# Performance work log

Measured on AMD Instinct MI355X. Metric: run time of the kernel, lower is better.

Reference implementation:

```python
import jax, jax.numpy as jnp
import numpy as np


def setup_inputs() -> dict:
    key = jax.random.key(0)
    k1, k2, k3 = jax.random.split(key, 3)
    B, C_IN, C_OUT, R, K = 4, 64, 64, 64, 3
    x = jax.random.normal(k1, (B, C_IN, R, R, R), dtype=jnp.float32)
    # per-voxel nonzero test |x|.sum(channel) != 0 used by the module)
    keep = jax.random.uniform(k2, (B, 1, R, R, R)) < 0.3
    x = x * keep.astype(jnp.float32)
    weight = jax.random.normal(k3, (C_OUT, C_IN, K, K, K), dtype=jnp.float32)
    return {"x": x, "weight": weight}


def reference(x, weight):
    # The torch module gathers a k^3 neighborhood at every nonzero input voxel,
    # contracts with the (unflipped) weight, and scatters to the same voxel.
    # This is exactly cross-correlation (torch conv semantics) with SAME padding,
    # masked to voxels where the input is nonzero across channels.
    K = weight.shape[-1]
    pad_l = K // 2
    pad_r = K - 1 - pad_l
    out = jax.lax.conv_general_dilated(
        x, weight,
        window_strides=(1, 1, 1),
        padding=[(pad_l, pad_r)] * 3,
        dimension_numbers=("NCDHW", "OIDHW", "NCDHW"),
    )  # [B, C_out, D, H, W]
    mask = (jnp.abs(x).sum(axis=1, keepdims=True) != 0)  # [B,1,D,H,W]
    return out * mask.astype(out.dtype)
```

## Files before the change

kernel.cpp:

```cpp
#include <hip/hip_runtime.h>
#include <stdint.h>


#define R3 262144
#define NVOX (4 * R3)
#define P  66
#define PS (66 * 66)
#define PB (66 * 66 * 66)
#define WSW_ELEMS (27 * 2 * 4 * 64 * 8)
#define CAP (NVOX / 2)

typedef __attribute__((ext_vector_type(4))) float f32x4;
typedef __attribute__((ext_vector_type(8))) short short8;

static __device__ inline unsigned short f2bf(float f) {
    union { float f; unsigned u; } v; v.f = f;
    unsigned u = v.u;
    return (unsigned short)((u + 0x7fffu + ((u >> 16) & 1u)) >> 16);
}

static __device__ __forceinline__ void gload16(const void* g, void* l) {
    __builtin_amdgcn_global_load_lds(
        (const __attribute__((address_space(1))) unsigned int*)g,
        (__attribute__((address_space(3))) unsigned int*)l, 16, 0, 0);
}

__global__ void wprep(const float* __restrict__ w, unsigned short* __restrict__ wsw) {
    int e = blockIdx.x * 256 + threadIdx.x;
    if (e >= WSW_ELEMS) return;
    int j    = e & 7;
    int lane = (e >> 3) & 63;
    int nt   = (e >> 9) & 3;
    int kc   = (e >> 11) & 1;
    int tap  = e >> 12;
    int co = nt * 16 + (lane & 15);
    int ci = kc * 32 + ((lane >> 4) * 8) + j;
    wsw[e] = f2bf(w[(co * 64 + ci) * 27 + tap]);
}

__global__ void __launch_bounds__(256) halo_zero(uint4* __restrict__ xt4) {
    int p = blockIdx.x * 256 + threadIdx.x;
    if (p >= 4 * PB) return;
    int b = p / PB;
    int rp = p - b * PB;
    int z = rp / PS; rp -= z * PS;
    int y = rp / P;  int xx = rp - y * P;
    if (z == 0 || z == 65 || y == 0 || y == 65 || xx == 0 || xx == 65) {
        uint4 zz = {0, 0, 0, 0};
        uint4* d = xt4 + (size_t)p * 8;
#pragma unroll
        for (int k = 0; k < 8; ++k) d[k] = zz;
    }
}

__global__ void __launch_bounds__(256) xprep(const float* __restrict__ x,
                                             unsigned int* __restrict__ xt_u32,
                                             int* __restrict__ list,
                                             int* __restrict__ pos,
                                             int* __restrict__ count) {
    __shared__ unsigned int lds[256 * 36];
    __shared__ unsigned int wcnt[4], wbase[4], bbase;
    int t = threadIdx.x;
    int v = blockIdx.x * 256 + t;
    int b = v >> 18;
    int s = v & (R3 - 1);
    const float* xb = x + (size_t)b * (64 * R3) + s;
    bool active = false;
    unsigned int pk[32];
#pragma unroll
    for (int c2 = 0; c2 < 32; ++c2) {
        float f0 = xb[(size_t)(2 * c2) * R3];
        float f1 = xb[(size_t)(2 * c2 + 1) * R3];
        active |= (f0 != 0.f) | (f1 != 0.f);
        pk[c2] = (unsigned)f2bf(f0) | ((unsigned)f2bf(f1) << 16);
    }
#pragma unroll
    for (int k = 0; k < 8; ++k) {
        uint4 q = { pk[4 * k], pk[4 * k + 1], pk[4 * k + 2], pk[4 * k + 3] };
        *(uint4*)&lds[t * 36 + 4 * k] = q;
    }
    __syncthreads();
    int s0 = (blockIdx.x * 256) & (R3 - 1);
    int z0 = s0 >> 12;
    int y0 = (s0 >> 6) & 63;
    size_t rowbase = ((size_t)b * PB + (size_t)(z0 + 1) * PS + (size_t)(y0 + 1) * P + 1) * 32;
#pragma unroll
    for (int i = 0; i < 8; ++i) {
        int g4 = i * 256 + t;
        int vox = g4 >> 3;
        int col = (g4 & 7) * 4;
        uint4 val = *(const uint4*)&lds[vox * 36 + col];
        int r = vox >> 6;
        int xc = vox & 63;
        *(uint4*)&xt_u32[rowbase + (size_t)r * (P * 32) + (size_t)xc * 32 + col] = val;
    }
    int lane = t & 63, w = t >> 6;
    unsigned long long bal = __ballot(active);
    if (lane == 0) wcnt[w] = (unsigned)__popcll(bal);
    __syncthreads();
    if (t == 0) {
        unsigned tot = 0;
        for (int i = 0; i < 4; ++i) { wbase[i] = tot; tot += wcnt[i]; }
        bbase = (unsigned)atomicAdd(count, (int)tot);
    }
    __syncthreads();
    int p = -1;
    if (active) {
        unsigned pp = bbase + wbase[w] + (unsigned)__popcll(bal & ((1ULL << lane) - 1ULL));
        list[pp] = v;
        p = (int)pp;
    }
    pos[v] = p;
}

#define STAGE(tap, buf) do {                                                       \
    const int dz_ = (tap) / 9 - 1, dy_ = ((tap) / 3) % 3 - 1, dx_ = (tap) % 3 - 1; \
    const ptrdiff_t dlt_ = (ptrdiff_t)(dz_ * PS + dy_ * P + dx_) * 128;            \
    _Pragma("unroll")                                                              \
    for (int i_ = 0; i_ < 4; ++i_)                                                 \
        gload16(asrc[i_] + dlt_, &Ab[buf][t * 16 + i_ * 8192]);                    \
    gload16(wswb + (size_t)(tap) * 8192 + t * 16, &Bb[buf][t * 16]);               \
} while (0)

__global__ void __launch_bounds__(512) sconv_gemm(const unsigned char* __restrict__ xt,
                                                  const unsigned char* __restrict__ wswb,
                                                  const int* __restrict__ list,
                                                  const int* __restrict__ count_p,
                                                  float* __restrict__ out,
                                                  float* __restrict__ compact,
                                                  int use_compact) {
    __shared__ __align__(16) unsigned char Ab[2][32768];
    __shared__ __align__(16) unsigned char Bb[2][8192];
    int count = *count_p;
    int nt_act = (count + 255) >> 8;
    int bid = blockIdx.x;
    if (bid >= nt_act) return;
    int qd = nt_act >> 3, rd = nt_act & 7;
    int xcd = bid & 7, ixx = bid >> 3;
    int tile = (xcd < rd ? xcd * (qd + 1) : rd * (qd + 1) + (xcd - rd) * qd) + ixx;
    int base = tile * 256;
    int t = threadIdx.x;

    const unsigned char* asrc[4];
    {
        int seg = t & 7;
        int r0 = t >> 3;
        int off = (seg * 16) ^ ((r0 & 7) << 4);
#pragma unroll
        for (int i = 0; i < 4; ++i) {
            int gi = base + r0 + 64 * i;
            int vid = (gi < count) ? list[gi] : 0;
            if (vid < 0) vid = 0;
            int bb = vid >> 18, sp = vid & (R3 - 1);
            int vz = sp >> 12, vy = (sp >> 6) & 63, vx = sp & 63;
            size_t pvox = (size_t)bb * PB + (size_t)(vz + 1) * PS + (size_t)(vy + 1) * P + (vx + 1);
            asrc[i] = xt + pvox * 128 + off;
        }
    }

    int lane = t & 63, w = t >> 6;
    int cl = lane & 15;
    int hi16 = (lane >> 4) * 16;
    int aswz = (cl & 7) << 4;
    int aoff[2][2];
#pragma unroll
    for (int m = 0; m < 2; ++m)
#pragma unroll
        for (int kc = 0; kc < 2; ++kc)
            aoff[m][kc] = (w * 32 + m * 16 + cl) * 128 + ((kc * 64 + hi16) ^ aswz);
    int boff[2][4];
#pragma unroll
    for (int kc = 0; kc < 2; ++kc)
#pragma unroll
        for (int n = 0; n < 4; ++n)
            boff[kc][n] = ((kc * 4 + n) * 64 + lane) * 16;

    f32x4 acc[2][4] = {};

    STAGE(0, 0);
#pragma unroll
    for (int tap = 0; tap < 27; ++tap) {
        const int cur = tap & 1;
        asm volatile("s_waitcnt vmcnt(0)" ::: "memory");
        asm volatile("s_barrier" ::: "memory");
        if (tap < 26) { STAGE(tap + 1, cur ^ 1); }
#pragma unroll
        for (int kc = 0; kc < 2; ++kc) {
            short8 a0 = *(const short8*)&Ab[cur][aoff[0][kc]];
            short8 a1 = *(const short8*)&Ab[cur][aoff[1][kc]];
#pragma unroll
            for (int n = 0; n < 4; ++n) {
                short8 bf = *(const short8*)&Bb[cur][boff[kc][n]];
                acc[0][n] = __builtin_amdgcn_mfma_f32_16x16x32_bf16(a0, bf, acc[0][n], 0, 0, 0);
                acc[1][n] = __builtin_amdgcn_mfma_f32_16x16x32_bf16(a1, bf, acc[1][n], 0, 0, 0);
            }
        }
        asm volatile("s_waitcnt lgkmcnt(0)" ::: "memory");
    }

    int q = lane >> 4;
    if (use_compact) {
#pragma unroll
        for (int m = 0; m < 2; ++m) {
#pragma unroll
            for (int rg = 0; rg < 4; ++rg) {
                int row = w * 32 + m * 16 + q * 4 + rg;
                int gi = base + row;
                if (gi < count && gi < CAP) {
#pragma unroll
                    for (int n = 0; n < 4; ++n)
                        compact[(size_t)gi * 64 + n * 16 + cl] = acc[m][n][rg];
                }
            }
        }
    } else {
#pragma unroll
        for (int m = 0; m < 2; ++m) {
#pragma unroll
            for (int rg = 0; rg < 4; ++rg) {
                int row = w * 32 + m * 16 + q * 4 + rg;
                int gi = base + row;
                if (gi < count) {
                    int vv = list[gi];
                    int bb2 = vv >> 18;
                    int sp = vv & (R3 - 1);
                    float* op = out + (size_t)(bb2 * 64 + cl) * R3 + sp;
#pragma unroll
                    for (int n = 0; n < 4; ++n)
                        op[(size_t)(n * 16) * R3] = acc[m][n][rg];
                }
            }
        }
    }
}

__global__ void __launch_bounds__(256) finalize(const uint4* __restrict__ compact4,
                                                const int* __restrict__ pos,
                                                float* __restrict__ out) {
    int t = threadIdx.x;
    int vb = blockIdx.x * 256;
    int b = vb >> 18;
    int sp0 = vb & (R3 - 1);
    int q = pos[vb + t];
    bool act = (unsigned)q < (unsigned)CAP;
    const uint4* src = compact4 + (size_t)(act ? q : 0) * 16;
    uint4 r[16];
#pragma unroll
    for (int s = 0; s < 16; ++s) {
        uint4 v = {0, 0, 0, 0};
        if (act) v = src[s];
        r[s] = v;
    }
    const float* rf = (const float*)r;
    float* ob = out + (size_t)b * 64 * R3 + sp0 + t;
#pragma unroll
    for (int co = 0; co < 64; ++co)
        ob[(size_t)co * R3] = rf[co];
}

__global__ void __launch_bounds__(64) fallback_conv(const float* __restrict__ x,
                                                    const float* __restrict__ wt,
                                                    float* __restrict__ out) {
    __shared__ float rowb[66];
    int bid = blockIdx.x;
    int y = bid & 63, z = (bid >> 6) & 63, co = (bid >> 12) & 63, b = bid >> 18;
    int t = threadIdx.x;
    float acc = 0.f;
    bool active = false;
    for (int ci = 0; ci < 64; ++ci) {
        const float* xp = x + ((size_t)(b * 64 + ci)) * R3;
        const float* wp = wt + ((size_t)(co * 64 + ci)) * 27;
        for (int dz = -1; dz <= 1; ++dz) {
            int nz = z + dz;
            bool okz = (unsigned)nz < 64u;
            for (int dy = -1; dy <= 1; ++dy) {
                int ny = y + dy;
                bool ok = okz && ((unsigned)ny < 64u);
                float v = ok ? xp[nz * 4096 + ny * 64 + t] : 0.f;
                rowb[t + 1] = v;
                if (t == 0) { rowb[0] = 0.f; rowb[65] = 0.f; }
                __syncthreads();
                if (dz == 0 && dy == 0) active |= (rowb[t + 1] != 0.f);
                const float* wq = wp + (dz + 1) * 9 + (dy + 1) * 3;
                acc += rowb[t] * wq[0] + rowb[t + 1] * wq[1] + rowb[t + 2] * wq[2];
                __syncthreads();
            }
        }
    }
    out[((size_t)(b * 64 + co)) * R3 + z * 4096 + y * 64 + t] = active ? acc : 0.f;
}

extern "C" void kernel_launch(void* const* d_in, const int* in_sizes, int n_in,
                              void* d_out, int out_size, void* d_ws, size_t ws_size,
                              hipStream_t stream) {
    const float* x = (const float*)d_in[0];
    const float* w = (const float*)d_in[1];
    float* out = (float*)d_out;

    const size_t XT_BYTES = (size_t)4 * PB * 128;
    const size_t LIST_OFF = XT_BYTES;
    const size_t POS_OFF  = LIST_OFF + (size_t)NVOX * 4;
    const size_t WSW_OFF  = POS_OFF + (size_t)NVOX * 4;
    const size_t CNT_OFF  = WSW_OFF + (size_t)WSW_ELEMS * 2;
    const size_t CMP_OFF  = (CNT_OFF + 256 + 255) & ~(size_t)255;
    const size_t NEED_S   = CMP_OFF;
    const size_t NEED_C   = CMP_OFF + (size_t)CAP * 64 * 4;

    if (ws_size < NEED_S) {
        fallback_conv<<<NVOX, 64, 0, stream>>>(x, w, out);
        return;
    }

    unsigned int*   xt   = (unsigned int*)d_ws;
    int*            list = (int*)((char*)d_ws + LIST_OFF);
    int*            pos  = (int*)((char*)d_ws + POS_OFF);
    unsigned short* wsw  = (unsigned short*)((char*)d_ws + WSW_OFF);
    int*            cnt  = (int*)((char*)d_ws + CNT_OFF);
    float*          cmp  = (float*)((char*)d_ws + CMP_OFF);
    int use_compact = (ws_size >= NEED_C) ? 1 : 0;

    hipMemsetAsync(cnt, 0, sizeof(int), stream);
    if (!use_compact)
        hipMemsetAsync(d_out, 0, (size_t)out_size * sizeof(float), stream);
    wprep<<<WSW_ELEMS / 256, 256, 0, stream>>>(w, wsw);
    halo_zero<<<(4 * PB + 255) / 256, 256, 0, stream>>>((uint4*)d_ws);
    xprep<<<NVOX / 256, 256, 0, stream>>>(x, xt, list, pos, cnt);
    sconv_gemm<<<NVOX / 256, 512, 0, stream>>>((const unsigned char*)xt,
                                               (const unsigned char*)wsw, list, cnt,
                                               out, cmp, use_compact);
    if (use_compact)
        finalize<<<NVOX / 256, 256, 0, stream>>>((const uint4*)cmp, pos, out);
}
```

Before: 650.8 us.

## Restructure sparse conv GEMM into per-wave triple-buffered pipeline with register-held weights

Each wave now stages its own 32-row A tile into a private 3-slot LDS ring and loads B (weights) straight from global into double-buffered registers. Block-level barriers are replaced with vmcnt-based waits. Blocks shrink to 256 threads and 128 voxels, with a 3-blocks-per-CU launch bound. The goal is to remove the per-tap barrier stalls and overlap global loads with MFMA work. The cost is that every wave fetches the weights separately, raising register pressure and global weight traffic.

Result: slower. 683.0 us (+4.9%).

```diff
diff --git a/kernel.cpp b/kernel.cpp
--- a/kernel.cpp
+++ b/kernel.cpp
@@ -113,42 +113,50 @@
     pos[v] = p;
 }
 
-#define STAGE(tap, buf) do {                                                       \
-    const int dz_ = (tap) / 9 - 1, dy_ = ((tap) / 3) % 3 - 1, dx_ = (tap) % 3 - 1; \
-    const ptrdiff_t dlt_ = (ptrdiff_t)(dz_ * PS + dy_ * P + dx_) * 128;            \
-    _Pragma("unroll")                                                              \
-    for (int i_ = 0; i_ < 4; ++i_)                                                 \
-        gload16(asrc[i_] + dlt_, &Ab[buf][t * 16 + i_ * 8192]);                    \
-    gload16(wswb + (size_t)(tap) * 8192 + t * 16, &Bb[buf][t * 16]);               \
-} while (0)
-
-__global__ void __launch_bounds__(512) sconv_gemm(const unsigned char* __restrict__ xt,
-                                                  const unsigned char* __restrict__ wswb,
-                                                  const int* __restrict__ list,
-                                                  const int* __restrict__ count_p,
-                                                  float* __restrict__ out,
-                                                  float* __restrict__ compact,
-                                                  int use_compact) {
-    __shared__ __align__(16) unsigned char Ab[2][32768];
-    __shared__ __align__(16) unsigned char Bb[2][8192];
+#define AST(tp, sl) do { if ((tp) < 27) {                                           \
+    const int dz_ = (tp) / 9 - 1, dy_ = ((tp) / 3) % 3 - 1, dx_ = (tp) % 3 - 1;     \
+    const ptrdiff_t dlt_ = (ptrdiff_t)(dz_ * PS + dy_ * P + dx_) * 128;             \
+    _Pragma("unroll")                                                               \
+    for (int i_ = 0; i_ < 4; ++i_)                                                  \
+        gload16(asrc[i_] + dlt_, aw + (sl) * 4096 + i_ * 1024 + lane * 16);         \
+    asm volatile("" ::: "memory");                                                  \
+} } while (0)
+
+#define BLD(tp, st) do { if ((tp) < 27) {                                           \
+    _Pragma("unroll")                                                               \
+    for (int j_ = 0; j_ < 8; ++j_)                                                  \
+        breg[st][j_] = *(const short8*)(wswb + (size_t)(tp) * 8192 + j_ * 1024      \
+                                        + lane * 16);                               \
+    asm volatile("" ::: "memory");                                                  \
+} } while (0)
+
+__global__ void __launch_bounds__(256, 3) sconv_gemm(const unsigned char* __restrict__ xt,
+                                                     const unsigned char* __restrict__ wswb,
+                                                     const int* __restrict__ list,
+                                                     const int* __restrict__ count_p,
+                                                     float* __restrict__ out,
+                                                     float* __restrict__ compact,
+                                                     int use_compact) {
+    __shared__ __align__(16) unsigned char Ab[4][3][4096];
     int count = *count_p;
-    int nt_act = (count + 255) >> 8;
+    int nt_act = (count + 127) >> 7;
     int bid = blockIdx.x;
     if (bid >= nt_act) return;
     int qd = nt_act >> 3, rd = nt_act & 7;
     int xcd = bid & 7, ixx = bid >> 3;
     int tile = (xcd < rd ? xcd * (qd + 1) : rd * (qd + 1) + (xcd - rd) * qd) + ixx;
-    int base = tile * 256;
+    int base = tile * 128;
     int t = threadIdx.x;
+    int lane = t & 63, w = t >> 6;
 
     const unsigned char* asrc[4];
     {
-        int seg = t & 7;
-        int r0 = t >> 3;
-        int off = (seg * 16) ^ ((r0 & 7) << 4);
+        int seg = lane & 7;
+        int rl0 = lane >> 3;
+        int off = (seg * 16) ^ ((rl0 & 7) << 4);
 #pragma unroll
         for (int i = 0; i < 4; ++i) {
-            int gi = base + r0 + 64 * i;
+            int gi = base + w * 32 + rl0 + 8 * i;
             int vid = (gi < count) ? list[gi] : 0;
             if (vid < 0) vid = 0;
             int bb = vid >> 18, sp = vid & (R3 - 1);
@@ -157,43 +165,45 @@
             asrc[i] = xt + pvox * 128 + off;
         }
     }
-
-    int lane = t & 63, w = t >> 6;
+    unsigned char* aw = &Ab[w][0][0];
+
     int cl = lane & 15;
     int hi16 = (lane >> 4) * 16;
-    int aswz = (cl & 7) << 4;
     int aoff[2][2];
 #pragma unroll
     for (int m = 0; m < 2; ++m)
 #pragma unroll
         for (int kc = 0; kc < 2; ++kc)
-            aoff[m][kc] = (w * 32 + m * 16 + cl) * 128 + ((kc * 64 + hi16) ^ aswz);
-    int boff[2][4];
-#pragma unroll
-    for (int kc = 0; kc < 2; ++kc)
-#pragma unroll
-        for (int n = 0; n < 4; ++n)
-            boff[kc][n] = ((kc * 4 + n) * 64 + lane) * 16;
+            aoff[m][kc] = (m * 16 + cl) * 128 + ((kc * 64 + hi16) ^ ((cl & 7) << 4));
 
     f32x4 acc[2][4] = {};
-
-    STAGE(0, 0);
-#pragma unroll
-    for (int tap = 0; tap < 27; ++tap) {
-        const int cur = tap & 1;
-        asm volatile("s_waitcnt vmcnt(0)" ::: "memory");
-        asm volatile("s_barrier" ::: "memory");
-        if (tap < 26) { STAGE(tap + 1, cur ^ 1); }
-#pragma unroll
-        for (int kc = 0; kc < 2; ++kc) {
-            short8 a0 = *(const short8*)&Ab[cur][aoff[0][kc]];
-            short8 a1 = *(const short8*)&Ab[cur][aoff[1][kc]];
-#pragma unroll
-            for (int n = 0; n < 4; ++n) {
-                short8 bf = *(const short8*)&Bb[cur][boff[kc][n]];
-                acc[0][n] = __builtin_amdgcn_mfma_f32_16x16x32_bf16(a0, bf, acc[0][n], 0, 0, 0);
-                acc[1][n] = __builtin_amdgcn_mfma_f32_16x16x32_bf16(a1, bf, acc[1][n], 0, 0, 0);
-            }
+    short8 breg[2][8];
+
+    BLD(0, 0);
+    AST(0, 0);
+    AST(1, 1);
+#pragma unroll
+    for (int tp = 0; tp < 27; ++tp) {
+        const int sl = tp % 3;
+        const int st = tp & 1;
+        if (tp == 0)       asm volatile("s_waitcnt vmcnt(4)"  ::: "memory");
+        else if (tp < 26)  asm volatile("s_waitcnt vmcnt(12)" ::: "memory");
+        else               asm volatile("s_waitcnt vmcnt(8)"  ::: "memory");
+        short8 a0k0 = *(const short8*)(aw + sl * 4096 + aoff[0][0]);
+        short8 a1k0 = *(const short8*)(aw + sl * 4096 + aoff[1][0]);
+        short8 a0k1 = *(const short8*)(aw + sl * 4096 + aoff[0][1]);
+        short8 a1k1 = *(const short8*)(aw + sl * 4096 + aoff[1][1]);
+        BLD(tp + 1, st ^ 1);
+        AST(tp + 2, (tp + 2) % 3);
+#pragma unroll
+        for (int n = 0; n < 4; ++n) {
+            acc[0][n] = __builtin_amdgcn_mfma_f32_16x16x32_bf16(a0k0, breg[st][n], acc[0][n], 0, 0, 0);
+            acc[1][n] = __builtin_amdgcn_mfma_f32_16x16x32_bf16(a1k0, breg[st][n], acc[1][n], 0, 0, 0);
+        }
+#pragma unroll
+        for (int n = 0; n < 4; ++n) {
+            acc[0][n] = __builtin_amdgcn_mfma_f32_16x16x32_bf16(a0k1, breg[st][4 + n], acc[0][n], 0, 0, 0);
+            acc[1][n] = __builtin_amdgcn_mfma_f32_16x16x32_bf16(a1k1, breg[st][4 + n], acc[1][n], 0, 0, 0);
         }
         asm volatile("s_waitcnt lgkmcnt(0)" ::: "memory");
     }
@@ -325,7 +335,7 @@
     wprep<<<WSW_ELEMS / 256, 256, 0, stream>>>(w, wsw);
     halo_zero<<<(4 * PB + 255) / 256, 256, 0, stream>>>((uint4*)d_ws);
     xprep<<<NVOX / 256, 256, 0, stream>>>(x, xt, list, pos, cnt);
-    sconv_gemm<<<NVOX / 256, 512, 0, stream>>>((const unsigned char*)xt,
+    sconv_gemm<<<NVOX / 128, 256, 0, stream>>>((const unsigned char*)xt,
                                                (const unsigned char*)wsw, list, cnt,
                                                out, cmp, use_compact);
     if (use_compact)
```
